# Optimization experiments

Measured on AMD Instinct MI355X. Metric: run time of the kernel, lower is better.

## Reference

```python
import jax, jax.numpy as jnp
import numpy as np

N_NODES = 100000
N_EDGES = 1600000
NUM_GRAPHS = 512
NUM_CLASSES = 16


def gcn_conv(x, src, dst, W, b, n):
    # PyG GCNConv: h = x @ W; add self-loops; symmetric norm D^-1/2 A D^-1/2; + bias
    h = x @ W  # [N, out]
    loops = jnp.arange(n, dtype=src.dtype)
    s = jnp.concatenate([src, loops])
    d = jnp.concatenate([dst, loops])
    deg = jax.ops.segment_sum(jnp.ones_like(d, dtype=h.dtype), d, num_segments=n)
    dinv = jnp.where(deg > 0, jax.lax.rsqrt(deg), 0.0)
    norm = dinv[s] * dinv[d]  # [E+N]
    msgs = h[s] * norm[:, None]  # gather + scale (irregular access)
    out = jax.ops.segment_sum(msgs, d, num_segments=n)
    return out + b


def global_mean_pool(x, batch, num_graphs):
    sums = jax.ops.segment_sum(x, batch, num_segments=num_graphs)
    cnts = jax.ops.segment_sum(jnp.ones((x.shape[0],), x.dtype), batch, num_segments=num_graphs)
    return sums / jnp.maximum(cnts, 1.0)[:, None]


def setup_inputs() -> dict:
    key = jax.random.key(0)
    ks = jax.random.split(key, 12)
    x = jax.random.normal(ks[0], (N_NODES, 13), dtype=jnp.float32)
    edge_index = jax.random.randint(ks[1], (2, N_EDGES), 0, N_NODES, dtype=jnp.int64)
    batch = jnp.sort(jax.random.randint(ks[2], (N_NODES,), 0, NUM_GRAPHS, dtype=jnp.int64))

    def glorot(k, fin, fout):
        lim = np.sqrt(6.0 / (fin + fout)).astype(np.float32)
        return jax.random.uniform(k, (fin, fout), jnp.float32, -lim, lim)

    W1 = glorot(ks[3], 13, 16); b1 = jnp.zeros((16,), jnp.float32)
    W2 = glorot(ks[4], 16, 64); b2 = jnp.zeros((64,), jnp.float32)
    W3 = glorot(ks[5], 64, 128); b3 = jnp.zeros((128,), jnp.float32)
    Wl = glorot(ks[6], 128, NUM_CLASSES); bl = jnp.zeros((NUM_CLASSES,), jnp.float32)
    return {"x": x, "edge_index": edge_index, "batch": batch,
            "W1": W1, "b1": b1, "W2": W2, "b2": b2,
            "W3": W3, "b3": b3, "Wl": Wl, "bl": bl}


def reference(x, edge_index, batch, W1, b1, W2, b2, W3, b3, Wl, bl):
    n = x.shape[0]
    src, dst = edge_index[0], edge_index[1]
    h = jax.nn.relu(gcn_conv(x, src, dst, W1, b1, n))
    h = jax.nn.relu(gcn_conv(h, src, dst, W2, b2, n))
    h = jax.nn.relu(gcn_conv(h, src, dst, W3, b3, n))
    g = global_mean_pool(h, batch, NUM_GRAPHS)  # [G, 128]
    # dropout p=0.025 is identity in eval mode
    logits = g @ Wl + bl
    return jax.nn.log_softmax(logits, axis=1)
```

## Files before the change

### kernel.cpp

```cpp
#include <hip/hip_runtime.h>
#include <hip/hip_fp16.h>

#define NN 100000
#define NE 1600000
#define NG 512
#define NC 16
#define NBUK 391
#define EPB 8192
#define NB1 196

static inline int cdiv(long long a, int b) { return (int)((a + b - 1) / b); }

typedef __attribute__((ext_vector_type(2))) float floatx2;

__device__ __forceinline__ unsigned int pack_f16(float x, float y) {
  __half2 h = __floats2half2_rn(x, y);
  return *reinterpret_cast<unsigned int*>(&h);
}
__device__ __forceinline__ float2 unpack_f16(unsigned int u) {
  __half2 h = *reinterpret_cast<__half2*>(&u);
  return __half22float2(h);
}
__device__ __forceinline__ void acc8(float* acc, uint4 r) {
  float2 p0 = unpack_f16(r.x), p1 = unpack_f16(r.y);
  float2 p2 = unpack_f16(r.z), p3 = unpack_f16(r.w);
  acc[0] += p0.x; acc[1] += p0.y; acc[2] += p1.x; acc[3] += p1.y;
  acc[4] += p2.x; acc[5] += p2.y; acc[6] += p3.x; acc[7] += p3.y;
}
__device__ __forceinline__ void accf8(float* acc, unsigned int u) {
  floatx2 lo = __builtin_amdgcn_cvt_pk_f32_fp8(u, false);
  floatx2 hi = __builtin_amdgcn_cvt_pk_f32_fp8(u, true);
  acc[0] += lo.x; acc[1] += lo.y; acc[2] += hi.x; acc[3] += hi.y;
}

__global__ void k_zero_i(int* p, int n) {
  int i = blockIdx.x * blockDim.x + threadIdx.x;
  if (i < n) p[i] = 0;
}

__global__ void k_p1a(const int* __restrict__ dst, int* __restrict__ bcnt) {
  __shared__ int sh[NBUK];
  int t = threadIdx.x, blk = blockIdx.x;
  for (int u = t; u < NBUK; u += 256) sh[u] = 0;
  __syncthreads();
  int e0 = blk * EPB;
#pragma unroll
  for (int k = 0; k < EPB / 256; ++k) {
    int e = e0 + k * 256 + t;
    if (e < NE) atomicAdd(&sh[dst[e] >> 8], 1);
  }
  __syncthreads();
  for (int u = t; u < NBUK; u += 256) bcnt[u * NB1 + blk] = sh[u];
}

__global__ void k_p1b(const int* __restrict__ src, const int* __restrict__ dst,
                      const int* __restrict__ bpos, unsigned int* __restrict__ packed) {
  __shared__ int sbase[NBUK];
  int t = threadIdx.x, blk = blockIdx.x;
  for (int u = t; u < NBUK; u += 256) sbase[u] = bpos[u * NB1 + blk];
  __syncthreads();
  int e0 = blk * EPB;
#pragma unroll
  for (int k = 0; k < EPB / 256; ++k) {
    int e = e0 + k * 256 + t;
    if (e < NE) {
      int d = dst[e];
      int pos = atomicAdd(&sbase[d >> 8], 1);
      packed[pos] = ((unsigned int)(d & 255) << 24) | (unsigned int)src[e];
    }
  }
}

__global__ void k_p2(const unsigned int* __restrict__ packed, const int* __restrict__ bpos,
                     int* __restrict__ count, int* __restrict__ offs,
                     float* __restrict__ dinv, int* __restrict__ csr) {
  __shared__ int sh[256], sc[256], cur[256];
  int t = threadIdx.x, u = blockIdx.x;
  int s0 = bpos[u * NB1];
  int s1 = (u + 1 < NBUK) ? bpos[(u + 1) * NB1] : NE;
  sh[t] = 0;
  __syncthreads();
  for (int e = s0 + t; e < s1; e += 256) atomicAdd(&sh[packed[e] >> 24], 1);
  __syncthreads();
  sc[t] = sh[t];
  __syncthreads();
  for (int d = 1; d < 256; d <<= 1) {
    int a = (t >= d) ? sc[t - d] : 0;
    __syncthreads();
    sc[t] += a;
    __syncthreads();
  }
  int excl = sc[t] - sh[t];
  int node = u * 256 + t;
  if (node < NN) {
    count[node] = sh[t];
    offs[node] = s0 + excl;
    dinv[node] = rsqrtf((float)(sh[t] + 1));
  }
  cur[t] = s0 + excl;
  __syncthreads();
  for (int e = s0 + t; e < s1; e += 256) {
    unsigned int p = packed[e];
    int pos = atomicAdd(&cur[p >> 24], 1);
    csr[pos] = (int)(p & 0x00FFFFFFu);
  }
}

__global__ void k_bounds(const int* __restrict__ batch, int* __restrict__ gstart) {
  int i = blockIdx.x * blockDim.x + threadIdx.x;
  if (i > NN) return;
  int b = (i < NN) ? batch[i] : NG;
  int bp = (i > 0) ? batch[i - 1] : -1;
  for (int g = bp + 1; g <= b; ++g) gstart[g] = i;
}

__global__ void k_scan1(const int* __restrict__ in, int* __restrict__ out,
                        int* __restrict__ bsum, int n) {
  __shared__ int s[256];
  int t = threadIdx.x, i = blockIdx.x * 256 + t;
  int v = (i < n) ? in[i] : 0;
  s[t] = v;
  __syncthreads();
  for (int d = 1; d < 256; d <<= 1) {
    int a = (t >= d) ? s[t - d] : 0;
    __syncthreads();
    s[t] += a;
    __syncthreads();
  }
  if (i < n) out[i] = s[t] - v;
  if (t == 255) bsum[blockIdx.x] = s[255];
}

__global__ void k_scan2(const int* __restrict__ in, int* __restrict__ out, int nb) {
  __shared__ int s[512];
  int t = threadIdx.x;
  int v = (t < nb) ? in[t] : 0;
  s[t] = v;
  __syncthreads();
  for (int d = 1; d < 512; d <<= 1) {
    int a = (t >= d) ? s[t - d] : 0;
    __syncthreads();
    s[t] += a;
    __syncthreads();
  }
  if (t < nb) out[t] = s[t] - v;
}

__global__ void k_scan3b(int* __restrict__ a, const int* __restrict__ bpref, int n) {
  int i = blockIdx.x * blockDim.x + threadIdx.x;
  if (i < n) a[i] += bpref[i >> 8];
}

template <bool BR, bool PSOUT>
__global__ void k_agg16h(const unsigned int* __restrict__ h, const int* __restrict__ csr,
                         const int* __restrict__ offs, const int* __restrict__ count,
                         const float* __restrict__ dinv, const float* __restrict__ bias,
                         unsigned int* __restrict__ out) {
  int wave = threadIdx.x >> 6, lane = threadIdx.x & 63;
  int i = (blockIdx.x * 4 + wave) * 32 + (lane >> 1);
  int q = lane & 1;
  if (i >= NN) return;
  int off = offs[i], cnt = count[i];
  float di = dinv[i];
  float acc[8] = {0.f, 0.f, 0.f, 0.f, 0.f, 0.f, 0.f, 0.f};
  int j = 0;
  for (; j + 7 < cnt; j += 8) {
    int s0 = csr[off + j], s1 = csr[off + j + 1];
    int s2 = csr[off + j + 2], s3 = csr[off + j + 3];
    int s4 = csr[off + j + 4], s5 = csr[off + j + 5];
    int s6 = csr[off + j + 6], s7 = csr[off + j + 7];
    uint4 r0 = ((const uint4*)(h + (size_t)s0 * 8))[q];
    uint4 r1 = ((const uint4*)(h + (size_t)s1 * 8))[q];
    uint4 r2 = ((const uint4*)(h + (size_t)s2 * 8))[q];
    uint4 r3 = ((const uint4*)(h + (size_t)s3 * 8))[q];
    uint4 r4 = ((const uint4*)(h + (size_t)s4 * 8))[q];
    uint4 r5 = ((const uint4*)(h + (size_t)s5 * 8))[q];
    uint4 r6 = ((const uint4*)(h + (size_t)s6 * 8))[q];
    uint4 r7 = ((const uint4*)(h + (size_t)s7 * 8))[q];
    acc8(acc, r0); acc8(acc, r1); acc8(acc, r2); acc8(acc, r3);
    acc8(acc, r4); acc8(acc, r5); acc8(acc, r6); acc8(acc, r7);
  }
  for (; j < cnt; ++j) {
    uint4 r0 = ((const uint4*)(h + (size_t)csr[off + j] * 8))[q];
    acc8(acc, r0);
  }
  uint4 rs = ((const uint4*)(h + (size_t)i * 8))[q];
  acc8(acc, rs);
  float v[8];
#pragma unroll
  for (int t = 0; t < 8; ++t) {
    v[t] = acc[t] * di;
    if (BR) v[t] = fmaxf(v[t] + bias[q * 8 + t], 0.f);
    if (PSOUT) v[t] *= di;
  }
  uint4 o;
  o.x = pack_f16(v[0], v[1]);
  o.y = pack_f16(v[2], v[3]);
  o.z = pack_f16(v[4], v[5]);
  o.w = pack_f16(v[6], v[7]);
  ((uint4*)(out + (size_t)i * 8))[q] = o;
}

__global__ void k_agg_b64f8(const unsigned int* __restrict__ h, const int* __restrict__ csr,
                            const int* __restrict__ offs, const int* __restrict__ count,
                            const float* __restrict__ dinv, unsigned int* __restrict__ out) {
  int wave = threadIdx.x >> 6, lane = threadIdx.x & 63;
  int i = (blockIdx.x * 4 + wave) * 16 + (lane >> 2);
  int q = lane & 3;
  if (i >= NN) return;
  int off = offs[i], cnt = count[i];
  float di = dinv[i];
  float acc[16];
#pragma unroll
  for (int t = 0; t < 16; ++t) acc[t] = 0.f;
  int j = 0;
  for (; j + 3 < cnt; j += 4) {
    int s0 = csr[off + j], s1 = csr[off + j + 1];
    int s2 = csr[off + j + 2], s3 = csr[off + j + 3];
    uint4 r0 = ((const uint4*)(h + (size_t)s0 * 16))[q];
    uint4 r1 = ((const uint4*)(h + (size_t)s1 * 16))[q];
    uint4 r2 = ((const uint4*)(h + (size_t)s2 * 16))[q];
    uint4 r3 = ((const uint4*)(h + (size_t)s3 * 16))[q];
#define DEC16(r)                                                            \
  {                                                                         \
    accf8(acc + 0, r.x);                                                    \
    accf8(acc + 4, r.y);                                                    \
    accf8(acc + 8, r.z);                                                    \
    accf8(acc + 12, r.w);                                                   \
  }
    DEC16(r0) DEC16(r1) DEC16(r2) DEC16(r3)
  }
  for (; j < cnt; ++j) {
    uint4 r0 = ((const uint4*)(h + (size_t)csr[off + j] * 16))[q];
    DEC16(r0)
  }
  uint4 rs = ((const uint4*)(h + (size_t)i * 16))[q];
  DEC16(rs)
#undef DEC16
  uint4 o0, o1;
  o0.x = pack_f16(acc[0] * di, acc[1] * di);
  o0.y = pack_f16(acc[2] * di, acc[3] * di);
  o0.z = pack_f16(acc[4] * di, acc[5] * di);
  o0.w = pack_f16(acc[6] * di, acc[7] * di);
  o1.x = pack_f16(acc[8] * di, acc[9] * di);
  o1.y = pack_f16(acc[10] * di, acc[11] * di);
  o1.z = pack_f16(acc[12] * di, acc[13] * di);
  o1.w = pack_f16(acc[14] * di, acc[15] * di);
  uint4* dst = (uint4*)(out + (size_t)i * 32 + q * 8);
  dst[0] = o0;
  dst[1] = o1;
}

__global__ void k_dense1_h(const float* __restrict__ x, const float* __restrict__ W,
                           const float* __restrict__ dinv, unsigned int* __restrict__ out,
                           int n) {
  __shared__ float sW[13 * 16];
  for (int t = threadIdx.x; t < 13 * 16; t += blockDim.x) sW[t] = W[t];
  __syncthreads();
  int idx = blockIdx.x * blockDim.x + threadIdx.x;
  int i = idx >> 3, u = idx & 7;
  if (i >= n) return;
  float a0 = 0.f, a1 = 0.f;
#pragma unroll
  for (int k = 0; k < 13; ++k) {
    float av = x[(size_t)i * 13 + k];
    a0 += av * sW[k * 16 + 2 * u];
    a1 += av * sW[k * 16 + 2 * u + 1];
  }
  float di = dinv[i];
  out[(size_t)i * 8 + u] = pack_f16(a0 * di, a1 * di);
}

__global__ void k_dense2_f8(const unsigned int* __restrict__ a, const float* __restrict__ W,
                            const float* __restrict__ b, const float* __restrict__ dinv,
                            unsigned int* __restrict__ out, int n) {
  __shared__ float sW[16 * 64];
  __shared__ float sb[64];
  for (int t = threadIdx.x; t < 16 * 64; t += blockDim.x) sW[t] = W[t];
  for (int t = threadIdx.x; t < 64; t += blockDim.x) sb[t] = b[t];
  __syncthreads();
  int idx = blockIdx.x * blockDim.x + threadIdx.x;
  int i = idx >> 4, g4 = idx & 15;
  if (i >= n) return;
  float av[16];
#pragma unroll
  for (int u = 0; u < 8; ++u) {
    float2 p = unpack_f16(a[(size_t)i * 8 + u]);
    av[2 * u] = p.x;
    av[2 * u + 1] = p.y;
  }
  float acc[4];
#pragma unroll
  for (int ko = 0; ko < 4; ++ko) acc[ko] = sb[4 * g4 + ko];
#pragma unroll
  for (int k = 0; k < 16; ++k) {
#pragma unroll
    for (int ko = 0; ko < 4; ++ko) acc[ko] += av[k] * sW[k * 64 + 4 * g4 + ko];
  }
  float di = dinv[i];
#pragma unroll
  for (int ko = 0; ko < 4; ++ko) acc[ko] = fmaxf(acc[ko], 0.f) * di;
  unsigned int u = 0;
  u = __builtin_amdgcn_cvt_pk_fp8_f32(acc[0], acc[1], u, false);
  u = __builtin_amdgcn_cvt_pk_fp8_f32(acc[2], acc[3], u, true);
  out[(size_t)i * 16 + g4] = u;
}

#define P4_NPW 16
__global__ __launch_bounds__(256) void k_dense3_pool4(
    const unsigned int* __restrict__ t3h, const float* __restrict__ W3,
    const float* __restrict__ b3, const int* __restrict__ batch,
    float* __restrict__ gsum) {
  int wu = blockIdx.x * 4 + (threadIdx.x >> 6);
  int lane = threadIdx.x & 63;
  int run = wu >> 1;
  int o = (wu & 1) * 64 + lane;
  int n0 = run * P4_NPW;
  if (n0 >= NN) return;
  float wcol[64];
#pragma unroll
  for (int k = 0; k < 64; ++k) wcol[k] = W3[k * 128 + o];
  float bias = b3[o];
  float acc = 0.f;
  int curg = -1;
#pragma unroll 1
  for (int j = 0; j < P4_NPW; ++j) {
    int n = n0 + j;
    if (n >= NN) break;
    int nu = __builtin_amdgcn_readfirstlane(n);
    const uint4* row = (const uint4*)(t3h + (size_t)nu * 32);
    float v = bias;
#pragma unroll
    for (int q = 0; q < 8; ++q) {
      uint4 r = row[q];
      float2 p0 = unpack_f16(r.x), p1 = unpack_f16(r.y);
      float2 p2 = unpack_f16(r.z), p3 = unpack_f16(r.w);
      v += p0.x * wcol[8 * q] + p0.y * wcol[8 * q + 1] + p1.x * wcol[8 * q + 2] +
           p1.y * wcol[8 * q + 3] + p2.x * wcol[8 * q + 4] + p2.y * wcol[8 * q + 5] +
           p3.x * wcol[8 * q + 6] + p3.y * wcol[8 * q + 7];
    }
    int g = batch[nu];
    if (g != curg) {
      if (curg >= 0) atomicAdd(&gsum[curg * 128 + o], acc);
      curg = g;
      acc = 0.f;
    }
    acc += fmaxf(v, 0.f);
  }
  if (curg >= 0) atomicAdd(&gsum[curg * 128 + o], acc);
}

__global__ void k_head(const float* __restrict__ gsum, const int* __restrict__ gstart,
                       const float* __restrict__ Wl, const float* __restrict__ bl,
                       float* __restrict__ out) {
  int wave = threadIdx.x >> 6, lane = threadIdx.x & 63;
  int g = blockIdx.x * 4 + wave;
  if (g >= NG) return;
  int c = lane & 15, part = lane >> 4;
  float acc = 0.f;
#pragma unroll
  for (int kk = 0; kk < 32; ++kk) {
    int k = part * 32 + kk;
    acc += gsum[g * 128 + k] * Wl[k * NC + c];
  }
  acc += __shfl_xor(acc, 16);
  acc += __shfl_xor(acc, 32);
  int cnt = gstart[g + 1] - gstart[g];
  float inv = 1.0f / (float)max(cnt, 1);
  float logit = acc * inv + bl[c];
  float m = logit;
#pragma unroll
  for (int d = 1; d < 16; d <<= 1) m = fmaxf(m, __shfl_xor(m, d));
  float ex = expf(logit - m), s = ex;
#pragma unroll
  for (int d = 1; d < 16; d <<= 1) s += __shfl_xor(s, d);
  if (lane < 16) out[g * NC + lane] = logit - m - logf(s);
}

extern "C" void kernel_launch(void* const* d_in, const int* in_sizes, int n_in,
                              void* d_out, int out_size, void* d_ws, size_t ws_size,
                              hipStream_t stream) {
  const float* x = (const float*)d_in[0];
  const int* ei = (const int*)d_in[1];
  const int* batch = (const int*)d_in[2];
  const float* W1 = (const float*)d_in[3];
  const float* b1 = (const float*)d_in[4];
  const float* W2 = (const float*)d_in[5];
  const float* b2 = (const float*)d_in[6];
  const float* W3 = (const float*)d_in[7];
  const float* b3 = (const float*)d_in[8];
  const float* Wl = (const float*)d_in[9];
  const float* bl = (const float*)d_in[10];
  const int* src = ei;
  const int* dst = ei + NE;

  int* bcnt = (int*)d_ws;
  int* bsum = bcnt + NBUK * NB1;
  int* bpref = bsum + 1024;
  int* gstart = bpref + 1024;
  int* count = gstart + NG + 2;
  int* offs = count + NN;
  float* dinv = (float*)(offs + NN);
  float* gsum = (float*)(dinv + NN);
  unsigned int* packed = (unsigned int*)(gsum + NG * 128);
  int* csr = (int*)(packed + NE);
  unsigned int* t1p = (unsigned int*)(csr + NE);
  unsigned int* h1p = t1p + (size_t)NN * 8;
  unsigned int* t2p = h1p + (size_t)NN * 8;
  unsigned int* h2f8 = t2p + (size_t)NN * 8;
  unsigned int* t3h = h2f8 + (size_t)NN * 16;

  const int B = 256;
  const int NSC = NBUK * NB1;

  k_zero_i<<<cdiv(NG * 128, B), B, 0, stream>>>((int*)gsum, NG * 128);
  k_p1a<<<NB1, 256, 0, stream>>>(dst, bcnt);
  k_bounds<<<cdiv(NN + 1, B), B, 0, stream>>>(batch, gstart);
  k_scan1<<<cdiv(NSC, 256), 256, 0, stream>>>(bcnt, bcnt, bsum, NSC);
  k_scan2<<<1, 512, 0, stream>>>(bsum, bpref, cdiv(NSC, 256));
  k_scan3b<<<cdiv(NSC, B), B, 0, stream>>>(bcnt, bpref, NSC);
  k_p1b<<<NB1, 256, 0, stream>>>(src, dst, bcnt, packed);
  k_p2<<<NBUK, 256, 0, stream>>>(packed, bcnt, count, offs, dinv, csr);

  k_dense1_h<<<cdiv((long long)NN * 8, B), B, 0, stream>>>(x, W1, dinv, t1p, NN);
  k_agg16h<true, true><<<cdiv(NN, 128), B, 0, stream>>>(
      t1p, csr, offs, count, dinv, b1, h1p);
  k_agg16h<false, false><<<cdiv(NN, 128), B, 0, stream>>>(
      h1p, csr, offs, count, dinv, nullptr, t2p);
  k_dense2_f8<<<cdiv((long long)NN * 16, B), B, 0, stream>>>(t2p, W2, b2, dinv, h2f8, NN);
  k_agg_b64f8<<<cdiv(NN, 64), B, 0, stream>>>(h2f8, csr, offs, count, dinv, t3h);
  {
    int runs = cdiv(NN, P4_NPW);
    k_dense3_pool4<<<cdiv(runs * 2, 4), 256, 0, stream>>>(t3h, W3, b3, batch, gsum);
  }

  k_head<<<NG / 4, B, 0, stream>>>(gsum, gstart, Wl, bl, (float*)d_out);
}
```

Before: 192.4 us.

## Compute layer-3 dense transform with MFMA f16 and fuse mean-pool reduction

Replaces the scalar per-lane FMA dense3+pool kernel with one that uses MFMA 16x16x32 f16 instructions on 16-node tiles. A new prep kernel zeroes gsum and pre-packs W3 into f16 fragments in the MFMA B layout. Each wave then reduces the 16 rows with shuffles before doing atomics when all of them belong to one graph, and falls back to per-element atomics otherwise. W3 is now rounded to f16, which adds some precision loss, and the mixed-graph tiles issue more atomics.

```diff
diff --git a/kernel.cpp b/kernel.cpp
--- a/kernel.cpp
+++ b/kernel.cpp
@@ -12,6 +12,8 @@
 static inline int cdiv(long long a, int b) { return (int)((a + b - 1) / b); }
 
 typedef __attribute__((ext_vector_type(2))) float floatx2;
+typedef _Float16 half8_t __attribute__((ext_vector_type(8)));
+typedef float f32x4_t __attribute__((ext_vector_type(4)));
 
 __device__ __forceinline__ unsigned int pack_f16(float x, float y) {
   __half2 h = __floats2half2_rn(x, y);
@@ -32,10 +34,32 @@
   floatx2 hi = __builtin_amdgcn_cvt_pk_f32_fp8(u, true);
   acc[0] += lo.x; acc[1] += lo.y; acc[2] += hi.x; acc[3] += hi.y;
 }
+__device__ __forceinline__ half8_t as_h8(uint4 u) {
+  half8_t h;
+  __builtin_memcpy(&h, &u, 16);
+  return h;
+}
 
 __global__ void k_zero_i(int* p, int n) {
   int i = blockIdx.x * blockDim.x + threadIdx.x;
   if (i < n) p[i] = 0;
+}
+
+__global__ void k_prep(const float* __restrict__ W3, float* __restrict__ gsum,
+                       unsigned int* __restrict__ w3s) {
+  int b = blockIdx.x, t = threadIdx.x;
+  if (b < 256) {
+    gsum[b * 256 + t] = 0.f;
+    return;
+  }
+  int idx = (b - 256) * 256 + t;
+  int c = idx >> 7, kb = (idx >> 6) & 1, l = idx & 63;
+  int n = l & 15, kg = l >> 4;
+#pragma unroll
+  for (int j = 0; j < 4; ++j) {
+    int k0 = kb * 32 + kg * 8 + 2 * j;
+    w3s[idx * 4 + j] = pack_f16(W3[k0 * 128 + c * 16 + n], W3[(k0 + 1) * 128 + c * 16 + n]);
+  }
 }
 
 __global__ void k_p1a(const int* __restrict__ dst, int* __restrict__ bcnt) {
@@ -306,48 +330,54 @@
   out[(size_t)i * 16 + g4] = u;
 }
 
-#define P4_NPW 16
-__global__ __launch_bounds__(256) void k_dense3_pool4(
-    const unsigned int* __restrict__ t3h, const float* __restrict__ W3,
+__global__ __launch_bounds__(256) void k_d3pool_mfma(
+    const unsigned int* __restrict__ t3h, const unsigned int* __restrict__ w3s,
     const float* __restrict__ b3, const int* __restrict__ batch,
     float* __restrict__ gsum) {
   int wu = blockIdx.x * 4 + (threadIdx.x >> 6);
   int lane = threadIdx.x & 63;
-  int run = wu >> 1;
-  int o = (wu & 1) * 64 + lane;
-  int n0 = run * P4_NPW;
+  int n0 = wu * 16;
   if (n0 >= NN) return;
-  float wcol[64];
-#pragma unroll
-  for (int k = 0; k < 64; ++k) wcol[k] = W3[k * 128 + o];
-  float bias = b3[o];
-  float acc = 0.f;
-  int curg = -1;
-#pragma unroll 1
-  for (int j = 0; j < P4_NPW; ++j) {
-    int n = n0 + j;
-    if (n >= NN) break;
-    int nu = __builtin_amdgcn_readfirstlane(n);
-    const uint4* row = (const uint4*)(t3h + (size_t)nu * 32);
-    float v = bias;
-#pragma unroll
-    for (int q = 0; q < 8; ++q) {
-      uint4 r = row[q];
-      float2 p0 = unpack_f16(r.x), p1 = unpack_f16(r.y);
-      float2 p2 = unpack_f16(r.z), p3 = unpack_f16(r.w);
-      v += p0.x * wcol[8 * q] + p0.y * wcol[8 * q + 1] + p1.x * wcol[8 * q + 2] +
-           p1.y * wcol[8 * q + 3] + p2.x * wcol[8 * q + 4] + p2.y * wcol[8 * q + 5] +
-           p3.x * wcol[8 * q + 6] + p3.y * wcol[8 * q + 7];
+  uint4 bf[8][2];
+#pragma unroll
+  for (int c = 0; c < 8; ++c)
+#pragma unroll
+    for (int kb = 0; kb < 2; ++kb)
+      bf[c][kb] = ((const uint4*)w3s)[(c * 2 + kb) * 64 + lane];
+  const uint4* arow = (const uint4*)(t3h + (size_t)(n0 + (lane & 15)) * 32);
+  uint4 a0 = arow[lane >> 4];
+  uint4 a1 = arow[4 + (lane >> 4)];
+  f32x4_t acc[8];
+#pragma unroll
+  for (int c = 0; c < 8; ++c) {
+    f32x4_t z = {0.f, 0.f, 0.f, 0.f};
+    z = __builtin_amdgcn_mfma_f32_16x16x32_f16(as_h8(a0), as_h8(bf[c][0]), z, 0, 0, 0);
+    z = __builtin_amdgcn_mfma_f32_16x16x32_f16(as_h8(a1), as_h8(bf[c][1]), z, 0, 0, 0);
+    acc[c] = z;
+  }
+  float bias[8];
+#pragma unroll
+  for (int c = 0; c < 8; ++c) bias[c] = b3[c * 16 + (lane & 15)];
+  int gf = batch[n0], gl = batch[n0 + 15];
+  if (gf == gl) {
+#pragma unroll
+    for (int c = 0; c < 8; ++c) {
+      float s = fmaxf(acc[c][0] + bias[c], 0.f) + fmaxf(acc[c][1] + bias[c], 0.f) +
+                fmaxf(acc[c][2] + bias[c], 0.f) + fmaxf(acc[c][3] + bias[c], 0.f);
+      s += __shfl_xor(s, 16);
+      s += __shfl_xor(s, 32);
+      if (lane < 16) atomicAdd(&gsum[gf * 128 + c * 16 + lane], s);
     }
-    int g = batch[nu];
-    if (g != curg) {
-      if (curg >= 0) atomicAdd(&gsum[curg * 128 + o], acc);
-      curg = g;
-      acc = 0.f;
+  } else {
+#pragma unroll
+    for (int r = 0; r < 4; ++r) {
+      int g = batch[n0 + (lane >> 4) * 4 + r];
+#pragma unroll
+      for (int c = 0; c < 8; ++c)
+        atomicAdd(&gsum[g * 128 + c * 16 + (lane & 15)],
+                  fmaxf(acc[c][r] + bias[c], 0.f));
     }
-    acc += fmaxf(v, 0.f);
-  }
-  if (curg >= 0) atomicAdd(&gsum[curg * 128 + o], acc);
+  }
 }
 
 __global__ void k_head(const float* __restrict__ gsum, const int* __restrict__ gstart,
@@ -409,11 +439,12 @@
   unsigned int* t2p = h1p + (size_t)NN * 8;
   unsigned int* h2f8 = t2p + (size_t)NN * 8;
   unsigned int* t3h = h2f8 + (size_t)NN * 16;
+  unsigned int* w3s = t3h + (size_t)NN * 32;
 
   const int B = 256;
   const int NSC = NBUK * NB1;
 
-  k_zero_i<<<cdiv(NG * 128, B), B, 0, stream>>>((int*)gsum, NG * 128);
+  k_prep<<<260, 256, 0, stream>>>(W3, gsum, w3s);
   k_p1a<<<NB1, 256, 0, stream>>>(dst, bcnt);
   k_bounds<<<cdiv(NN + 1, B), B, 0, stream>>>(batch, gstart);
   k_scan1<<<cdiv(NSC, 256), 256, 0, stream>>>(bcnt, bcnt, bsum, NSC);
@@ -429,10 +460,7 @@
       h1p, csr, offs, count, dinv, nullptr, t2p);
   k_dense2_f8<<<cdiv((long long)NN * 16, B), B, 0, stream>>>(t2p, W2, b2, dinv, h2f8, NN);
   k_agg_b64f8<<<cdiv(NN, 64), B, 0, stream>>>(h2f8, csr, offs, count, dinv, t3h);
-  {
-    int runs = cdiv(NN, P4_NPW);
-    k_dense3_pool4<<<cdiv(runs * 2, 4), 256, 0, stream>>>(t3h, W3, b3, batch, gsum);
-  }
+  k_d3pool_mfma<<<cdiv(cdiv(NN, 16), 4), 256, 0, stream>>>(t3h, w3s, b3, batch, gsum);
 
   k_head<<<NG / 4, B, 0, stream>>>(gsum, gstart, Wl, bl, (float*)d_out);
 }
```

Measured after the change: 185.0 us. -3.9%, faster.
